# Kernel tuning notes

Measured on AMD Instinct MI355X. Metric: run time of the kernel, lower is better.

Reference implementation:

```python
import jax, jax.numpy as jnp
import numpy as np

DIM = 1024
NUM_HEADS = 16
HEAD_DIM = DIM // NUM_HEADS


def setup_inputs() -> dict:
    key = jax.random.key(0)
    ks = jax.random.split(key, 9)
    B, T, D = 4, 8192, DIM
    s = 1.0 / np.sqrt(D)
    return {
        "x": jax.random.normal(ks[0], (B, T, D), dtype=jnp.float32),
        "Wq": jax.random.normal(ks[1], (D, D), dtype=jnp.float32) * s,
        "bq": jnp.zeros((D,), dtype=jnp.float32),
        "Wk": jax.random.normal(ks[2], (D, D), dtype=jnp.float32) * s,
        "bk": jnp.zeros((D,), dtype=jnp.float32),
        "Wv": jax.random.normal(ks[3], (D, D), dtype=jnp.float32) * s,
        "bv": jnp.zeros((D,), dtype=jnp.float32),
        "Wo": jax.random.normal(ks[4], (D, D), dtype=jnp.float32) * s,
        "bo": jnp.zeros((D,), dtype=jnp.float32),
    }


def _feature_map(x):
    # elu(x) + 1
    return jax.nn.elu(x) + 1.0


def reference(x, Wq, bq, Wk, bk, Wv, bv, Wo, bo):
    B, T, D = x.shape
    H, hd = NUM_HEADS, HEAD_DIM
    q = (x @ Wq.T + bq).reshape(B, T, H, hd)
    k = (x @ Wk.T + bk).reshape(B, T, H, hd)
    v = (x @ Wv.T + bv).reshape(B, T, H, hd)
    q = _feature_map(q)
    k = _feature_map(k)
    eps = 1e-6
    kv = jnp.einsum('bthd,bthm->bhmd', k, v)      # [B,H,hd,hd]
    k_sum = k.sum(axis=1)                          # [B,H,hd]
    z = 1.0 / (jnp.einsum('bthd,bhd->bth', q, k_sum) + eps)
    out = jnp.einsum('bthd,bhmd->bthm', q, kv) * z[..., None]
    out = out.reshape(B, T, D)
    return out @ Wo.T + bo
```

## Files before the change

kernel.cpp:

```cpp
#include <hip/hip_runtime.h>
#include <stdint.h>

typedef __bf16 bf16x8 __attribute__((ext_vector_type(8)));
typedef float f32x4 __attribute__((ext_vector_type(4)));
typedef unsigned short u16x8 __attribute__((ext_vector_type(8)));
typedef unsigned short u16x4 __attribute__((ext_vector_type(4)));

#define MFMA16(a, b, c) __builtin_amdgcn_mfma_f32_16x16x32_bf16(a, b, c, 0, 0, 0)
#define BAR() __builtin_amdgcn_s_barrier()
#define LGK0() do { asm volatile("s_waitcnt lgkmcnt(0)" ::: "memory"); \
                    __builtin_amdgcn_sched_barrier(0); } while (0)
#define VMC(n) asm volatile("s_waitcnt vmcnt(" #n ")" ::: "memory")
#define PRIO(p) __builtin_amdgcn_s_setprio(p)

#define TSEQ 8192
#define BATCH 4

static __device__ __forceinline__ unsigned short f2bf(float f) {
  union { float f; unsigned u; } v; v.f = f;
  unsigned u = v.u + 0x7FFFu + ((v.u >> 16) & 1u);
  return (unsigned short)(u >> 16);
}
static __device__ __forceinline__ float bf2f(unsigned short h) {
  union { unsigned u; float f; } v; v.u = ((unsigned)h) << 16; return v.f;
}
static __device__ __forceinline__ void gload16(const void* g, void* l) {
  __builtin_amdgcn_global_load_lds((const __attribute__((address_space(1))) void*)g,
                                   (__attribute__((address_space(3))) void*)l, 16, 0, 0);
}

__global__ __launch_bounds__(256) void cvt_bf16(const float* __restrict__ s,
                                                unsigned short* __restrict__ d, int n) {
  int i = (blockIdx.x * 256 + threadIdx.x) * 8;
  if (i >= n) return;
  const float4 a = *(const float4*)(s + i);
  const float4 b = *(const float4*)(s + i + 4);
  u16x8 o;
  o[0] = f2bf(a.x); o[1] = f2bf(a.y); o[2] = f2bf(a.z); o[3] = f2bf(a.w);
  o[4] = f2bf(b.x); o[5] = f2bf(b.y); o[6] = f2bf(b.z); o[7] = f2bf(b.w);
  *(u16x8*)(d + i) = o;
}

__global__ __launch_bounds__(256) void cvt_weights(const float* __restrict__ wq,
                                                   const float* __restrict__ wk,
                                                   const float* __restrict__ wv,
                                                   const float* __restrict__ wo,
                                                   unsigned short* __restrict__ wcat,
                                                   unsigned short* __restrict__ wobf) {
  const int r = blockIdx.x >> 9;
  const float* s = (r == 0) ? wq : (r == 1) ? wk : (r == 2) ? wv : wo;
  unsigned short* d = (r < 3) ? (wcat + r * 1048576) : wobf;
  const int i = ((blockIdx.x & 511) * 256 + threadIdx.x) * 8;
  const float4 a = *(const float4*)(s + i);
  const float4 b = *(const float4*)(s + i + 4);
  u16x8 o;
  o[0] = f2bf(a.x); o[1] = f2bf(a.y); o[2] = f2bf(a.z); o[3] = f2bf(a.w);
  o[4] = f2bf(b.x); o[5] = f2bf(b.y); o[6] = f2bf(b.z); o[7] = f2bf(b.w);
  *(u16x8*)(d + i) = o;
}


static __device__ __forceinline__ void stage_half(const unsigned short* __restrict__ G,
                                                  int grow0, char* L, int t, int h,
                                                  int tid, int w) {
  #pragma unroll
  for (int j = 0; j < 2; ++j) {
    const int ci = j * 512 + tid;
    const int rr = ci >> 3;
    const int gch = (ci & 7) ^ (rr & 7);
    gload16(G + (size_t)(grow0 + h * 128 + rr) * 1024 + t * 64 + gch * 8,
            L + (t & 1) * 32768 + h * 16384 + j * 8192 + w * 1024);
  }
}

template <bool S1, bool S3, bool S4, int VM>
static __device__ __forceinline__ void tile_body(
    const unsigned short* __restrict__ A, const unsigned short* __restrict__ B,
    int rowA0, int rowB0, char* As, char* Bs, int t, f32x4 acc[8][4],
    int Abase, int Bbase, int tid, int w) {
  const int buf = (t & 1) * 32768;
  bf16x8 a0[4][2], a1[4][2], b0[2][2], b1[2][2];
  #pragma unroll
  for (int mf = 0; mf < 4; ++mf)
    #pragma unroll
    for (int ks = 0; ks < 2; ++ks)
      a0[mf][ks] = *(const bf16x8*)(As + ((buf + Abase + mf * 2048) ^ (ks << 6)));
  #pragma unroll
  for (int nf = 0; nf < 2; ++nf)
    #pragma unroll
    for (int ks = 0; ks < 2; ++ks)
      b0[nf][ks] = *(const bf16x8*)(Bs + ((buf + Bbase + nf * 2048) ^ (ks << 6)));
  if (S1) stage_half(A, rowA0, As, t + 1, 1, tid, w);
  BAR(); LGK0(); PRIO(1);
  #pragma unroll
  for (int mf = 0; mf < 4; ++mf)
    #pragma unroll
    for (int nf = 0; nf < 2; ++nf)
      #pragma unroll
      for (int ks = 0; ks < 2; ++ks)
        acc[mf][nf] = MFMA16(a0[mf][ks], b0[nf][ks], acc[mf][nf]);
  PRIO(0); BAR();
  #pragma unroll
  for (int nf = 0; nf < 2; ++nf)
    #pragma unroll
    for (int ks = 0; ks < 2; ++ks)
      b1[nf][ks] = *(const bf16x8*)(Bs + ((buf + Bbase + (nf + 2) * 2048) ^ (ks << 6)));
  BAR(); LGK0(); PRIO(1);
  #pragma unroll
  for (int mf = 0; mf < 4; ++mf)
    #pragma unroll
    for (int nf = 0; nf < 2; ++nf)
      #pragma unroll
      for (int ks = 0; ks < 2; ++ks)
        acc[mf][nf + 2] = MFMA16(a0[mf][ks], b1[nf][ks], acc[mf][nf + 2]);
  PRIO(0); BAR();
  #pragma unroll
  for (int mf = 0; mf < 4; ++mf)
    #pragma unroll
    for (int ks = 0; ks < 2; ++ks)
      a1[mf][ks] = *(const bf16x8*)(As + ((buf + Abase + (mf + 4) * 2048) ^ (ks << 6)));
  if (S3) {
    stage_half(B, rowB0, Bs, t + 2, 0, tid, w);
    stage_half(B, rowB0, Bs, t + 2, 1, tid, w);
  }
  BAR(); LGK0(); PRIO(1);
  #pragma unroll
  for (int mf = 0; mf < 4; ++mf)
    #pragma unroll
    for (int nf = 0; nf < 2; ++nf)
      #pragma unroll
      for (int ks = 0; ks < 2; ++ks)
        acc[mf + 4][nf + 2] = MFMA16(a1[mf][ks], b1[nf][ks], acc[mf + 4][nf + 2]);
  PRIO(0); BAR();
  if (S4) stage_half(A, rowA0, As, t + 2, 0, tid, w);
  if (VM == 6) { VMC(6); } else { VMC(0); }
  BAR(); PRIO(1);
  #pragma unroll
  for (int mf = 0; mf < 4; ++mf)
    #pragma unroll
    for (int nf = 0; nf < 2; ++nf)
      #pragma unroll
      for (int ks = 0; ks < 2; ++ks)
        acc[mf + 4][nf] = MFMA16(a1[mf][ks], b0[nf][ks], acc[mf + 4][nf]);
  PRIO(0); BAR();
}

static __device__ __forceinline__ void gemm256(const unsigned short* __restrict__ A,
                                               const unsigned short* __restrict__ B,
                                               int rowA0, int rowB0,
                                               char* As, char* Bs, f32x4 acc[8][4]) {
  const int tid = threadIdx.x, l = tid & 63, w = tid >> 6;
  const int wr = w >> 2, wc = w & 3;
  const int cp0 = (l >> 4) ^ (l & 7);
  const int Abase = (wr * 128 + (l & 15)) * 128 + cp0 * 16;
  const int Bbase = (wc * 64 + (l & 15)) * 128 + cp0 * 16;
  stage_half(A, rowA0, As, 0, 0, tid, w);
  stage_half(A, rowA0, As, 0, 1, tid, w);
  stage_half(B, rowB0, Bs, 0, 0, tid, w);
  stage_half(B, rowB0, Bs, 0, 1, tid, w);
  stage_half(B, rowB0, Bs, 1, 0, tid, w);
  stage_half(B, rowB0, Bs, 1, 1, tid, w);
  stage_half(A, rowA0, As, 1, 0, tid, w);
  VMC(6); BAR();
  #pragma unroll 1
  for (int t = 0; t < 14; ++t)
    tile_body<true, true, true, 6>(A, B, rowA0, rowB0, As, Bs, t, acc, Abase, Bbase, tid, w);
  tile_body<true, false, false, 0>(A, B, rowA0, rowB0, As, Bs, 14, acc, Abase, Bbase, tid, w);
  tile_body<false, false, false, 0>(A, B, rowA0, rowB0, As, Bs, 15, acc, Abase, Bbase, tid, w);
}

__global__ __launch_bounds__(512, 2) void qkv_gemm256(
    const unsigned short* __restrict__ xbf, const unsigned short* __restrict__ wcat,
    const float* __restrict__ bq, const float* __restrict__ bk, const float* __restrict__ bv,
    unsigned short* __restrict__ qout, unsigned short* __restrict__ kout,
    unsigned short* __restrict__ vout) {
  __shared__ char smem[131072];
  char* As = smem;
  char* Bs = smem + 65536;
  const int swz = (blockIdx.x & 7) * 192 + (blockIdx.x >> 3);
  const int mt = swz / 12, nt = swz % 12;
  f32x4 acc[8][4] = {};
  gemm256(xbf, wcat, mt * 256, nt * 256, As, Bs, acc);

  const int l = threadIdx.x & 63, w = threadIdx.x >> 6;
  const int wr = w >> 2, wc = w & 3;
  const int region = nt >> 2;
  const float* bias = (region == 0) ? bq : (region == 1) ? bk : bv;
  unsigned short* dst = (region == 0) ? qout : (region == 1) ? kout : vout;
  const int colb = (nt & 3) * 256 + wc * 64;
  #pragma unroll
  for (int mf = 0; mf < 8; ++mf) {
    #pragma unroll
    for (int nf = 0; nf < 4; ++nf) {
      const int col = colb + nf * 16 + (l & 15);
      const float bb = bias[col];
      #pragma unroll
      for (int j = 0; j < 4; ++j) {
        const int row = mt * 256 + wr * 128 + mf * 16 + (l >> 4) * 4 + j;
        float v = acc[mf][nf][j] + bb;
        if (region < 2) v = (v > 0.f) ? (v + 1.f) : __expf(v);
        dst[(size_t)row * 1024 + col] = f2bf(v);
      }
    }
  }
}

__global__ __launch_bounds__(512, 2) void o_gemm256(
    const unsigned short* __restrict__ attn, const unsigned short* __restrict__ wo,
    const float* __restrict__ bo, float* __restrict__ out) {
  __shared__ char smem[131072];
  char* As = smem;
  char* Bs = smem + 65536;
  const int swz = (blockIdx.x & 7) * 64 + (blockIdx.x >> 3);
  const int mt = swz >> 2, nt = swz & 3;
  f32x4 acc[8][4] = {};
  gemm256(attn, wo, mt * 256, nt * 256, As, Bs, acc);

  const int l = threadIdx.x & 63, w = threadIdx.x >> 6;
  const int wr = w >> 2, wc = w & 3;
  #pragma unroll
  for (int mf = 0; mf < 8; ++mf) {
    #pragma unroll
    for (int nf = 0; nf < 4; ++nf) {
      const int col = nt * 256 + wc * 64 + nf * 16 + (l & 15);
      const float bb = bo[col];
      #pragma unroll
      for (int j = 0; j < 4; ++j) {
        const int row = mt * 256 + wr * 128 + mf * 16 + (l >> 4) * 4 + j;
        out[(size_t)row * 1024 + col] = acc[mf][nf][j] + bb;
      }
    }
  }
}

__global__ __launch_bounds__(64) void kv_reduce(const unsigned short* __restrict__ kbf,
                                                const unsigned short* __restrict__ vbf,
                                                float* __restrict__ part) {
  const int bh = blockIdx.x, tc = blockIdx.y;
  const int b = bh >> 4, h = bh & 15;
  const int l = threadIdx.x;
  const int tm = l & 15, td = l >> 4;
  const unsigned short* kb = kbf + (size_t)b * TSEQ * 1024 + h * 64;
  const unsigned short* vb = vbf + (size_t)b * TSEQ * 1024 + h * 64;
  float acc[4][16] = {};
  float ksum = 0.f;
  const int t0 = tc * 256;
  #pragma unroll 2
  for (int t = t0; t < t0 + 256; ++t) {
    const unsigned short* krow = kb + (size_t)t * 1024;
    const unsigned short* vrow = vb + (size_t)t * 1024;
    const u16x8 k8a = *(const u16x8*)(krow + td * 16);
    const u16x8 k8b = *(const u16x8*)(krow + td * 16 + 8);
    const u16x4 v4 = *(const u16x4*)(vrow + tm * 4);
    float kf[16];
    #pragma unroll
    for (int j = 0; j < 8; ++j) { kf[j] = bf2f(k8a[j]); kf[8 + j] = bf2f(k8b[j]); }
    float vf[4];
    #pragma unroll
    for (int i = 0; i < 4; ++i) vf[i] = bf2f(v4[i]);
    ksum += bf2f(krow[td * 16 + tm]);
    #pragma unroll
    for (int i = 0; i < 4; ++i)
      #pragma unroll
      for (int j = 0; j < 16; ++j)
        acc[i][j] += vf[i] * kf[j];
  }
  float* ps = part + (size_t)(tc * 64 + bh) * 65 * 64;
  #pragma unroll
  for (int i = 0; i < 4; ++i) {
    const int m = tm * 4 + i;
    #pragma unroll
    for (int j = 0; j < 16; j += 4) {
      float4 o = make_float4(acc[i][j], acc[i][j + 1], acc[i][j + 2], acc[i][j + 3]);
      *(float4*)(ps + m * 64 + td * 16 + j) = o;
    }
  }
  ps[64 * 64 + td * 16 + tm] = ksum;
}

__global__ __launch_bounds__(256) void kv_finalize(const float* __restrict__ part,
                                                   unsigned short* __restrict__ bmat) {
  const int e = blockIdx.x * 256 + threadIdx.x;
  if (e >= 64 * 80 * 64) return;
  const int d = e & 63;
  const int r = (e >> 6) % 80;
  const int bh = e / (80 * 64);
  float s = 0.f;
  if (r < 65) {
    #pragma unroll
    for (int tc = 0; tc < 32; ++tc)
      s += part[((size_t)(tc * 64 + bh) * 65 + r) * 64 + d];
  }
  bmat[e] = f2bf(s);
}

__global__ __launch_bounds__(256) void attn_gemm(const unsigned short* __restrict__ qbf,
                                                 const unsigned short* __restrict__ bmat,
                                                 unsigned short* __restrict__ attn) {
  __shared__ char Qs[16384];
  __shared__ char Bs2[10240];
  const int bh = blockIdx.x, mt = blockIdx.y;
  const int b = bh >> 4, h = bh & 15;
  const int tid = threadIdx.x, l = tid & 63, w = tid >> 6;

  const unsigned short* qbase = qbf + (size_t)(b * TSEQ + mt * 128) * 1024 + h * 64;
  #pragma unroll
  for (int r4 = 0; r4 < 4; ++r4) {
    const int ci = r4 * 256 + tid;
    const int row = ci >> 3;
    const int csrc = (ci & 7) ^ (row & 7);
    gload16(qbase + (size_t)row * 1024 + csrc * 8, Qs + (r4 * 256 + w * 64) * 16);
  }
  const unsigned short* bbase = bmat + (size_t)bh * 80 * 64;
  #pragma unroll
  for (int r4 = 0; r4 < 3; ++r4) {
    const int ci = r4 * 256 + tid;
    if (ci < 640) {
      const int row = ci >> 3;
      const int csrc = (ci & 7) ^ (row & 7);
      gload16(bbase + row * 64 + csrc * 8, Bs2 + (r4 * 256 + w * 64) * 16);
    }
  }
  __syncthreads();

  f32x4 acc[2][5] = {};
  #pragma unroll
  for (int ks = 0; ks < 2; ++ks) {
    bf16x8 af[2], bfr[5];
    #pragma unroll
    for (int m = 0; m < 2; ++m) {
      const int r = w * 32 + m * 16 + (l & 15);
      const int c = ((l >> 4) + ks * 4) ^ (r & 7);
      af[m] = *(const bf16x8*)(Qs + r * 128 + c * 16);
    }
    #pragma unroll
    for (int n = 0; n < 5; ++n) {
      const int r = n * 16 + (l & 15);
      const int c = ((l >> 4) + ks * 4) ^ (r & 7);
      bfr[n] = *(const bf16x8*)(Bs2 + r * 128 + c * 16);
    }
    #pragma unroll
    for (int m = 0; m < 2; ++m)
      #pragma unroll
      for (int n = 0; n < 5; ++n)
        acc[m][n] = MFMA16(af[m], bfr[n], acc[m][n]);
  }

  unsigned short* arow = attn + (size_t)(b * TSEQ + mt * 128) * 1024 + h * 64;
  #pragma unroll
  for (int m = 0; m < 2; ++m) {
    #pragma unroll
    for (int j = 0; j < 4; ++j) {
      const float den = __shfl(acc[m][4][j], (l & 48));
      const float z = 1.f / (den + 1e-6f);
      const int row = w * 32 + m * 16 + (l >> 4) * 4 + j;
      #pragma unroll
      for (int n = 0; n < 4; ++n)
        arow[(size_t)row * 1024 + n * 16 + (l & 15)] = f2bf(acc[m][n][j] * z);
    }
  }
}

extern "C" void kernel_launch(void* const* d_in, const int* in_sizes, int n_in,
                              void* d_out, int out_size, void* d_ws, size_t ws_size,
                              hipStream_t stream) {
  const float* x  = (const float*)d_in[0];
  const float* Wq = (const float*)d_in[1];
  const float* bq = (const float*)d_in[2];
  const float* Wk = (const float*)d_in[3];
  const float* bk = (const float*)d_in[4];
  const float* Wv = (const float*)d_in[5];
  const float* bv = (const float*)d_in[6];
  const float* Wo = (const float*)d_in[7];
  const float* bo = (const float*)d_in[8];
  float* out = (float*)d_out;
  char* ws = (char*)d_ws;

  unsigned short* xbf  = (unsigned short*)(ws + 0);
  unsigned short* wcat = (unsigned short*)(ws + 67108864);
  unsigned short* wobf = (unsigned short*)(ws + 73400320);
  unsigned short* qbf  = (unsigned short*)(ws + 75497472);
  unsigned short* kbf  = (unsigned short*)(ws + 142606336);
  unsigned short* vbf  = (unsigned short*)(ws + 209715200);
  float* part          = (float*)(ws + 0);
  unsigned short* bmat = (unsigned short*)(ws + 34078720);
  unsigned short* attn = kbf;

  cvt_bf16<<<16384, 256, 0, stream>>>(x, xbf, 33554432);
  cvt_weights<<<2048, 256, 0, stream>>>(Wq, Wk, Wv, Wo, wcat, wobf);

  qkv_gemm256<<<1536, 512, 0, stream>>>(xbf, wcat, bq, bk, bv, qbf, kbf, vbf);
  kv_reduce<<<dim3(64, 32), 64, 0, stream>>>(kbf, vbf, part);
  kv_finalize<<<1280, 256, 0, stream>>>(part, bmat);
  attn_gemm<<<dim3(64, 64), 256, 0, stream>>>(qbf, bmat, attn);
  o_gemm256<<<512, 512, 0, stream>>>(attn, wobf, bo, out);
}
```

Measured before the change: 674.3 us.

## Prefetch next tile's LDS fragments across iterations and split kv_reduce finer

The GEMM inner loop now keeps the A and first-B fragments in registers across tiles. The next tile's fragments are read from LDS during the last MFMA phase, which removes one barrier/LDS-wait phase per tile, and the b0/b1 register roles are ping-ponged between tiles. Separately, kv_reduce splits the sequence into 64 chunks instead of 32 for more parallelism, with kv_finalize summing twice as many partials. The bmat workspace is moved to avoid overlapping the larger partials buffer. This adds register pressure and more partial-sum traffic.

```diff
diff --git a/kernel.cpp b/kernel.cpp
--- a/kernel.cpp
+++ b/kernel.cpp
@@ -73,57 +73,51 @@
   }
 }
 
-template <bool S1, bool S3, bool S4, int VM>
+template <bool S1, bool S3, bool S4, int VM, bool RD>
 static __device__ __forceinline__ void tile_body(
     const unsigned short* __restrict__ A, const unsigned short* __restrict__ B,
     int rowA0, int rowB0, char* As, char* Bs, int t, f32x4 acc[8][4],
+    bf16x8 (&a0)[4][2], bf16x8 (&b0)[2][2], bf16x8 (&b1)[2][2],
     int Abase, int Bbase, int tid, int w) {
   const int buf = (t & 1) * 32768;
-  bf16x8 a0[4][2], a1[4][2], b0[2][2], b1[2][2];
-  #pragma unroll
-  for (int mf = 0; mf < 4; ++mf)
-    #pragma unroll
-    for (int ks = 0; ks < 2; ++ks)
-      a0[mf][ks] = *(const bf16x8*)(As + ((buf + Abase + mf * 2048) ^ (ks << 6)));
-  #pragma unroll
-  for (int nf = 0; nf < 2; ++nf)
-    #pragma unroll
-    for (int ks = 0; ks < 2; ++ks)
-      b0[nf][ks] = *(const bf16x8*)(Bs + ((buf + Bbase + nf * 2048) ^ (ks << 6)));
-  if (S1) stage_half(A, rowA0, As, t + 1, 1, tid, w);
-  BAR(); LGK0(); PRIO(1);
-  #pragma unroll
-  for (int mf = 0; mf < 4; ++mf)
-    #pragma unroll
-    for (int nf = 0; nf < 2; ++nf)
-      #pragma unroll
-      for (int ks = 0; ks < 2; ++ks)
-        acc[mf][nf] = MFMA16(a0[mf][ks], b0[nf][ks], acc[mf][nf]);
-  PRIO(0); BAR();
+  const int nbuf = 32768 - buf;
+  bf16x8 a1[4][2];
   #pragma unroll
   for (int nf = 0; nf < 2; ++nf)
     #pragma unroll
     for (int ks = 0; ks < 2; ++ks)
       b1[nf][ks] = *(const bf16x8*)(Bs + ((buf + Bbase + (nf + 2) * 2048) ^ (ks << 6)));
-  BAR(); LGK0(); PRIO(1);
+  if (S1) stage_half(A, rowA0, As, t + 1, 1, tid, w);
+  PRIO(1);
   #pragma unroll
   for (int mf = 0; mf < 4; ++mf)
     #pragma unroll
     for (int nf = 0; nf < 2; ++nf)
       #pragma unroll
       for (int ks = 0; ks < 2; ++ks)
-        acc[mf][nf + 2] = MFMA16(a0[mf][ks], b1[nf][ks], acc[mf][nf + 2]);
-  PRIO(0); BAR();
+        acc[mf][nf] = MFMA16(a0[mf][ks], b0[nf][ks], acc[mf][nf]);
+  PRIO(0);
+  BAR();
   #pragma unroll
   for (int mf = 0; mf < 4; ++mf)
     #pragma unroll
     for (int ks = 0; ks < 2; ++ks)
       a1[mf][ks] = *(const bf16x8*)(As + ((buf + Abase + (mf + 4) * 2048) ^ (ks << 6)));
+  PRIO(1);
+  #pragma unroll
+  for (int mf = 0; mf < 4; ++mf)
+    #pragma unroll
+    for (int nf = 0; nf < 2; ++nf)
+      #pragma unroll
+      for (int ks = 0; ks < 2; ++ks)
+        acc[mf][nf + 2] = MFMA16(a0[mf][ks], b1[nf][ks], acc[mf][nf + 2]);
+  PRIO(0);
+  BAR();
   if (S3) {
     stage_half(B, rowB0, Bs, t + 2, 0, tid, w);
     stage_half(B, rowB0, Bs, t + 2, 1, tid, w);
   }
-  BAR(); LGK0(); PRIO(1);
+  PRIO(1);
   #pragma unroll
   for (int mf = 0; mf < 4; ++mf)
     #pragma unroll
@@ -131,18 +125,34 @@
       #pragma unroll
       for (int ks = 0; ks < 2; ++ks)
         acc[mf + 4][nf + 2] = MFMA16(a1[mf][ks], b1[nf][ks], acc[mf + 4][nf + 2]);
-  PRIO(0); BAR();
+  PRIO(0);
+  BAR();
   if (S4) stage_half(A, rowA0, As, t + 2, 0, tid, w);
-  if (VM == 6) { VMC(6); } else { VMC(0); }
-  BAR(); PRIO(1);
-  #pragma unroll
-  for (int mf = 0; mf < 4; ++mf)
+  if (VM == 6) { VMC(6); } else if (VM == 0) { VMC(0); }
+  if (VM >= 0) BAR();
+  if (RD) {
+    #pragma unroll
+    for (int mf = 0; mf < 4; ++mf)
+      #pragma unroll
+      for (int ks = 0; ks < 2; ++ks)
+        a0[mf][ks] = *(const bf16x8*)(As + ((nbuf + Abase + mf * 2048) ^ (ks << 6)));
     #pragma unroll
     for (int nf = 0; nf < 2; ++nf)
       #pragma unroll
       for (int ks = 0; ks < 2; ++ks)
+        b1[nf][ks] = *(const bf16x8*)(Bs + ((nbuf + Bbase + nf * 2048) ^ (ks << 6)));
+  }
+  PRIO(1);
+  #pragma unroll
+  for (int mf = 0; mf < 4; ++mf)
+    #pragma unroll
+    for (int nf = 0; nf < 2; ++nf)
+      #pragma unroll
+      for (int ks = 0; ks < 2; ++ks)
         acc[mf + 4][nf] = MFMA16(a1[mf][ks], b0[nf][ks], acc[mf + 4][nf]);
-  PRIO(0); BAR();
+  PRIO(0);
+  if (RD) LGK0();
+  BAR();
 }
 
 static __device__ __forceinline__ void gemm256(const unsigned short* __restrict__ A,
@@ -154,6 +164,7 @@
   const int cp0 = (l >> 4) ^ (l & 7);
   const int Abase = (wr * 128 + (l & 15)) * 128 + cp0 * 16;
   const int Bbase = (wc * 64 + (l & 15)) * 128 + cp0 * 16;
+  bf16x8 a0[4][2], bX[2][2], bY[2][2];
   stage_half(A, rowA0, As, 0, 0, tid, w);
   stage_half(A, rowA0, As, 0, 1, tid, w);
   stage_half(B, rowB0, Bs, 0, 0, tid, w);
@@ -162,11 +173,27 @@
   stage_half(B, rowB0, Bs, 1, 1, tid, w);
   stage_half(A, rowA0, As, 1, 0, tid, w);
   VMC(6); BAR();
+  #pragma unroll
+  for (int mf = 0; mf < 4; ++mf)
+    #pragma unroll
+    for (int ks = 0; ks < 2; ++ks)
+      a0[mf][ks] = *(const bf16x8*)(As + ((Abase + mf * 2048) ^ (ks << 6)));
+  #pragma unroll
+  for (int nf = 0; nf < 2; ++nf)
+    #pragma unroll
+    for (int ks = 0; ks < 2; ++ks)
+      bX[nf][ks] = *(const bf16x8*)(Bs + ((Bbase + nf * 2048) ^ (ks << 6)));
   #pragma unroll 1
-  for (int t = 0; t < 14; ++t)
-    tile_body<true, true, true, 6>(A, B, rowA0, rowB0, As, Bs, t, acc, Abase, Bbase, tid, w);
-  tile_body<true, false, false, 0>(A, B, rowA0, rowB0, As, Bs, 14, acc, Abase, Bbase, tid, w);
-  tile_body<false, false, false, 0>(A, B, rowA0, rowB0, As, Bs, 15, acc, Abase, Bbase, tid, w);
+  for (int i = 0; i < 7; ++i) {
+    tile_body<true, true, true, 6, true>(A, B, rowA0, rowB0, As, Bs, 2 * i, acc,
+                                         a0, bX, bY, Abase, Bbase, tid, w);
+    tile_body<true, true, true, 6, true>(A, B, rowA0, rowB0, As, Bs, 2 * i + 1, acc,
+                                         a0, bY, bX, Abase, Bbase, tid, w);
+  }
+  tile_body<true, false, false, 0, true>(A, B, rowA0, rowB0, As, Bs, 14, acc,
+                                         a0, bX, bY, Abase, Bbase, tid, w);
+  tile_body<false, false, false, -1, false>(A, B, rowA0, rowB0, As, Bs, 15, acc,
+                                            a0, bY, bX, Abase, Bbase, tid, w);
 }
 
 __global__ __launch_bounds__(512, 2) void qkv_gemm256(
@@ -244,9 +271,9 @@
   const unsigned short* vb = vbf + (size_t)b * TSEQ * 1024 + h * 64;
   float acc[4][16] = {};
   float ksum = 0.f;
-  const int t0 = tc * 256;
+  const int t0 = tc * 128;
   #pragma unroll 2
-  for (int t = t0; t < t0 + 256; ++t) {
+  for (int t = t0; t < t0 + 128; ++t) {
     const unsigned short* krow = kb + (size_t)t * 1024;
     const unsigned short* vrow = vb + (size_t)t * 1024;
     const u16x8 k8a = *(const u16x8*)(krow + td * 16);
@@ -288,7 +315,7 @@
   float s = 0.f;
   if (r < 65) {
     #pragma unroll
-    for (int tc = 0; tc < 32; ++tc)
+    for (int tc = 0; tc < 64; ++tc)
       s += part[((size_t)(tc * 64 + bh) * 65 + r) * 64 + d];
   }
   bmat[e] = f2bf(s);
@@ -383,14 +410,14 @@
   unsigned short* kbf  = (unsigned short*)(ws + 142606336);
   unsigned short* vbf  = (unsigned short*)(ws + 209715200);
   float* part          = (float*)(ws + 0);
-  unsigned short* bmat = (unsigned short*)(ws + 34078720);
+  unsigned short* bmat = (unsigned short*)(ws + 71303168);
   unsigned short* attn = kbf;
 
   cvt_bf16<<<16384, 256, 0, stream>>>(x, xbf, 33554432);
   cvt_weights<<<2048, 256, 0, stream>>>(Wq, Wk, Wv, Wo, wcat, wobf);
 
   qkv_gemm256<<<1536, 512, 0, stream>>>(xbf, wcat, bq, bk, bv, qbf, kbf, vbf);
-  kv_reduce<<<dim3(64, 32), 64, 0, stream>>>(kbf, vbf, part);
+  kv_reduce<<<dim3(64, 64), 64, 0, stream>>>(kbf, vbf, part);
   kv_finalize<<<1280, 256, 0, stream>>>(part, bmat);
   attn_gemm<<<dim3(64, 64), 256, 0, stream>>>(qbf, bmat, attn);
   o_gemm256<<<512, 512, 0, stream>>>(attn, wobf, bo, out);
```

New measurement: 946.3 us. 1.4x slower.
